# Performance work log

Hardware: AMD Instinct MI355X
Metric: run time of the kernel (lower is better)

## Reference

```python
import jax, jax.numpy as jnp
import numpy as np

TWO_PI = 2.0 * np.pi
VMIN, VMAX = 0.0, 255.0


def _reflect_idx(i, n):
    # TF fill_mode='reflect': (d c b a | a b c d | d c b a), i.e. mirror including edge
    m = jnp.mod(i, 2 * n)
    return jnp.where(m < n, m, 2 * n - 1 - m)


def _bilinear(img, sy, sx):
    # img: [H, W, C]; sy, sx: [H, W] float source coords
    H, W, _ = img.shape
    y0f = jnp.floor(sy)
    x0f = jnp.floor(sx)
    wy = (sy - y0f)[..., None]
    wx = (sx - x0f)[..., None]
    y0 = y0f.astype(jnp.int32)
    x0 = x0f.astype(jnp.int32)
    y0r = _reflect_idx(y0, H)
    y1r = _reflect_idx(y0 + 1, H)
    x0r = _reflect_idx(x0, W)
    x1r = _reflect_idx(x0 + 1, W)
    return (img[y0r, x0r] * (1 - wy) * (1 - wx)
            + img[y0r, x1r] * (1 - wy) * wx
            + img[y1r, x0r] * wy * (1 - wx)
            + img[y1r, x1r] * wy * wx)


def _affine_warp(img, a, b, c, d):
    # inverse map about image center: src = center + [[a,b],[c,d]] @ (dst - center)
    H, W, _ = img.shape
    cy = (H - 1) / 2.0
    cx = (W - 1) / 2.0
    y = jnp.arange(H, dtype=img.dtype)[:, None] - cy   # [H,1]
    x = jnp.arange(W, dtype=img.dtype)[None, :] - cx   # [1,W]
    sx = a * x + b * y + cx
    sy = c * x + d * y + cy
    return _bilinear(img, sy, sx)


def setup_inputs() -> dict:
    key = jax.random.key(0)
    k = jax.random.split(key, 7)
    B, H, W, C = 32, 512, 512, 3
    inputs = jax.random.uniform(k[0], (B, H, W, C), dtype=jnp.float32) * 255.0
    flip_h = jax.random.bernoulli(k[1], 0.5, (B,))
    flip_v = jax.random.bernoulli(k[2], 0.5, (B,))
    # RandomRotation(factor=0.5): angle in [-0.5, 0.5] * 2*pi
    angle = jax.random.uniform(k[3], (B,), jnp.float32, -0.5, 0.5) * TWO_PI
    # RandomZoom(height_factor=0.5, width_factor=None): isotropic zoom in [0.5, 1.5]
    zoom = jax.random.uniform(k[4], (B,), jnp.float32, 0.5, 1.5)
    # RandomBrightness(factor=0.5, value_range=(0,255)): delta in [-0.5, 0.5]*255
    delta = jax.random.uniform(k[5], (B,), jnp.float32, -0.5, 0.5) * 255.0
    # RandomContrast(factor=0.5): contrast multiplier in [0.5, 1.5]
    contrast = jax.random.uniform(k[6], (B,), jnp.float32, 0.5, 1.5)
    return {"inputs": inputs, "flip_h": flip_h, "flip_v": flip_v,
            "angle": angle, "zoom": zoom, "delta": delta, "contrast": contrast}


def reference(inputs, flip_h, flip_v, angle, zoom, delta, contrast):
    # 1) RandomFlip('horizontal_and_vertical'): independent per-image coin flips
    x = jnp.where(flip_h[:, None, None, None], inputs[:, :, ::-1, :], inputs)
    x = jnp.where(flip_v[:, None, None, None], x[:, ::-1, :, :], x)
    # 2) RandomRotation: bilinear warp, reflect fill
    cos = jnp.cos(angle)
    sin = jnp.sin(angle)
    x = jax.vmap(_affine_warp)(x, cos, -sin, sin, cos)
    # 3) RandomZoom (isotropic since width_factor=None): second bilinear warp
    zeros = jnp.zeros_like(zoom)
    x = jax.vmap(_affine_warp)(x, zoom, zeros, zeros, zoom)
    # 4) RandomBrightness: add per-image delta, clip to value_range
    x = jnp.clip(x + delta[:, None, None, None], VMIN, VMAX)
    # 5) RandomContrast: (x - per-channel mean) * f + mean, clip to value_range
    mean = jnp.mean(x, axis=(1, 2), keepdims=True)  # [B,1,1,C]
    x = jnp.clip((x - mean) * contrast[:, None, None, None] + mean, VMIN, VMAX)
    return x
```

## Files before the change

### kernel.cpp

```cpp
#include <hip/hip_runtime.h>


constexpr int Hh = 512, Ww = 512, Cc = 3, BATCH = 32;
constexpr int HW = Hh * Ww;
constexpr float CTR = 255.5f;
constexpr size_t IMG_FLOATS = (size_t)HW * Cc;

constexpr int TW = 64, TH = 16;
constexpr int RW = 99, RH = 26;
constexpr int KFILL = 10;

__device__ __forceinline__ int reflect1024(int i) {
    int m = i & 1023;
    return (m < 512) ? m : (1023 - m);
}

#define LOADPX(RX, RY, WX, WY, T00, T01, T10, T11)                              \
    {                                                                           \
        const int gx_ = reflect1024(rx0 + (int)(RX));                           \
        const int gy_ = reflect1024(ry0 + (int)(RY));                           \
        const float fx_ = (float)gx_ - CTR, fy_ = (float)gy_ - CTR;             \
                         \
        const float sx_ = cs * fx_ - sn * fy_ + CTR;                            \
        const float sy_ = sn * fx_ + cs * fy_ + CTR;                            \
        const float xf_ = floorf(sx_), yf_ = floorf(sy_);                       \
        (WX) = sx_ - xf_; (WY) = sy_ - yf_;                                     \
        const int xa_ = reflect1024((int)xf_)     ^ fhm;                        \
        const int xb_ = reflect1024((int)xf_ + 1) ^ fhm;                        \
        const int ya_ = reflect1024((int)yf_)     ^ fvm;                        \
        const int yb_ = reflect1024((int)yf_ + 1) ^ fvm;                        \
        (T00) = img[ya_ * Ww + xa_]; (T01) = img[ya_ * Ww + xb_];               \
        (T10) = img[yb_ * Ww + xa_]; (T11) = img[yb_ * Ww + xb_];               \
    }

#define STOREPX(RX, RY, WX, WY, T00, T01, T10, T11)                             \
    {                                                                           \
        const float w1y_ = 1.f - (WY), w1x_ = 1.f - (WX);                       \
        float3 o_;                                                              \
        o_.x = (((T00).x * w1y_) * w1x_) + (((T01).x * w1y_) * (WX))            \
             + (((T10).x * (WY)) * w1x_) + (((T11).x * (WY)) * (WX));           \
        o_.y = (((T00).y * w1y_) * w1x_) + (((T01).y * w1y_) * (WX))            \
             + (((T10).y * (WY)) * w1x_) + (((T11).y * (WY)) * (WX));           \
        o_.z = (((T00).z * w1y_) * w1x_) + (((T01).z * w1y_) * (WX))            \
             + (((T10).z * (WY)) * w1x_) + (((T11).z * (WY)) * (WX));           \
        lds[(RY)][(RX)] = o_;                                                   \
    }

__global__ __launch_bounds__(256, 4) void warp_fused(
    const float* __restrict__ in,
    const int* __restrict__ fh, const int* __restrict__ fv,
    const float* __restrict__ angle, const float* __restrict__ zoom,
    const float* __restrict__ delta,
    float* __restrict__ out, double* __restrict__ sums)
{
    __shared__ float3 lds[RH][RW];
    __shared__ float red[4][3];

    const int b = blockIdx.z;
    const float ang = angle[b];
    const float cs = cosf(ang), sn = sinf(ang);
    const float z  = zoom[b];
    const float dl = delta[b];
    const int fhm = fh[b] ? 511 : 0;
    const int fvm = fv[b] ? 511 : 0;
    const float3* __restrict__ img = (const float3*)(in + (size_t)b * IMG_FLOATS);
    float* __restrict__ outb = out + (size_t)b * IMG_FLOATS;

    const int X0 = blockIdx.x * TW;
    const int Y0 = blockIdx.y * TH;

    const int rx0 = (int)floorf(z * ((float)X0 - CTR) + CTR);
    const int ry0 = (int)floorf(z * ((float)Y0 - CTR) + CTR);
    const int rx1 = (int)floorf(z * ((float)(X0 + TW - 1) - CTR) + CTR) + 1;
    const int ry1 = (int)floorf(z * ((float)(Y0 + TH - 1) - CTR) + CTR) + 1;
    const unsigned Wr = (unsigned)(rx1 - rx0 + 1);
    const unsigned Hr = (unsigned)(ry1 - ry0 + 1);
    const unsigned N  = Wr * Hr;

    {
        unsigned i  = threadIdx.x;
        unsigned ry = i / Wr;
        unsigned rx = i - ry * Wr;
        const unsigned q = 256u / Wr;
        const unsigned r = 256u - q * Wr;

        bool cv = (i < N);
        unsigned crx = rx, cry = ry;
        float cwx, cwy; float3 c00, c01, c10, c11;
        if (cv) LOADPX(crx, cry, cwx, cwy, c00, c01, c10, c11);

        #pragma unroll
        for (int t = 1; t <= KFILL; ++t) {
            i += 256u;
            rx += r; ry += q;
            if (rx >= Wr) { rx -= Wr; ry += 1u; }
            const bool nv = (t < KFILL) && (i < N);
            unsigned nrx = rx, nry = ry;
            float nwx, nwy; float3 n00, n01, n10, n11;
            if (nv) LOADPX(nrx, nry, nwx, nwy, n00, n01, n10, n11);
            if (cv) STOREPX(crx, cry, cwx, cwy, c00, c01, c10, c11);
            cv = nv; crx = nrx; cry = nry; cwx = nwx; cwy = nwy;
            c00 = n00; c01 = n01; c10 = n10; c11 = n11;
        }
    }
    __syncthreads();

    const int tx  = threadIdx.x & 63;
    const int ty0 = threadIdx.x >> 6;
    const float sx = z * ((float)(X0 + tx) - CTR) + CTR;
    const float xf = floorf(sx);
    const float wx = sx - xf;
    const int lxa = (int)xf - rx0;
    const float w1x = 1.f - wx;

    float s0 = 0.f, s1 = 0.f, s2 = 0.f;
    #pragma unroll
    for (int k = 0; k < 4; ++k) {
        const int y = Y0 + ty0 + (k << 2);
        const float sy = z * ((float)y - CTR) + CTR;
        const float yf = floorf(sy);
        const float wy = sy - yf;
        const int lya = (int)yf - ry0;
        const float w1y = 1.f - wy;
        const float3 a0 = lds[lya][lxa],     a1 = lds[lya][lxa + 1];
        const float3 b0 = lds[lya + 1][lxa], b1 = lds[lya + 1][lxa + 1];
        float3 t;
        t.x = ((a0.x * w1y) * w1x) + ((a1.x * w1y) * wx)
            + ((b0.x * wy) * w1x)  + ((b1.x * wy) * wx);
        t.y = ((a0.y * w1y) * w1x) + ((a1.y * w1y) * wx)
            + ((b0.y * wy) * w1x)  + ((b1.y * wy) * wx);
        t.z = ((a0.z * w1y) * w1x) + ((a1.z * w1y) * wx)
            + ((b0.z * wy) * w1x)  + ((b1.z * wy) * wx);
        t.x = fminf(fmaxf(t.x + dl, 0.f), 255.f);
        t.y = fminf(fmaxf(t.y + dl, 0.f), 255.f);
        t.z = fminf(fmaxf(t.z + dl, 0.f), 255.f);
        *(float3*)(outb + (size_t)((y << 9) + X0 + tx) * 3) = t;
        s0 += t.x; s1 += t.y; s2 += t.z;
    }

    #pragma unroll
    for (int off = 32; off > 0; off >>= 1) {
        s0 += __shfl_down(s0, off);
        s1 += __shfl_down(s1, off);
        s2 += __shfl_down(s2, off);
    }
    const int lane = threadIdx.x & 63, wid = threadIdx.x >> 6;
    if (lane == 0) { red[wid][0] = s0; red[wid][1] = s1; red[wid][2] = s2; }
    __syncthreads();
    if (threadIdx.x == 0) {
        atomicAdd(&sums[b * 3 + 0], (double)red[0][0] + red[1][0] + red[2][0] + red[3][0]);
        atomicAdd(&sums[b * 3 + 1], (double)red[0][1] + red[1][1] + red[2][1] + red[3][1]);
        atomicAdd(&sums[b * 3 + 2], (double)red[0][2] + red[1][2] + red[2][2] + red[3][2]);
    }
}

__global__ __launch_bounds__(256) void contrast_pass(
    float* __restrict__ out, const double* __restrict__ sums,
    const float* __restrict__ contrast)
{
    const int b = blockIdx.y;
    const float f = contrast[b];
    const double invN = 1.0 / (double)HW;
    const float m0 = (float)(sums[b * 3 + 0] * invN);
    const float m1 = (float)(sums[b * 3 + 1] * invN);
    const float m2 = (float)(sums[b * 3 + 2] * invN);
    float4* base = reinterpret_cast<float4*>(out + (size_t)b * IMG_FLOATS);

    #pragma unroll
    for (int it = 0; it < 4; ++it) {
        const int i4 = it * 49152 + blockIdx.x * 256 + threadIdx.x;
        float4 v = base[i4];
        int c = (int)(((unsigned)i4 * 4u) % 3u);
        float m;
        m = (c == 0) ? m0 : ((c == 1) ? m1 : m2);
        v.x = fminf(fmaxf((v.x - m) * f + m, 0.f), 255.f); c = (c == 2) ? 0 : c + 1;
        m = (c == 0) ? m0 : ((c == 1) ? m1 : m2);
        v.y = fminf(fmaxf((v.y - m) * f + m, 0.f), 255.f); c = (c == 2) ? 0 : c + 1;
        m = (c == 0) ? m0 : ((c == 1) ? m1 : m2);
        v.z = fminf(fmaxf((v.z - m) * f + m, 0.f), 255.f); c = (c == 2) ? 0 : c + 1;
        m = (c == 0) ? m0 : ((c == 1) ? m1 : m2);
        v.w = fminf(fmaxf((v.w - m) * f + m, 0.f), 255.f);
        base[i4] = v;
    }
}

extern "C" void kernel_launch(void* const* d_in, const int* in_sizes, int n_in,
                              void* d_out, int out_size, void* d_ws, size_t ws_size,
                              hipStream_t stream) {
    const float* in       = (const float*)d_in[0];
    const int*   fh       = (const int*)d_in[1];
    const int*   fv       = (const int*)d_in[2];
    const float* angle    = (const float*)d_in[3];
    const float* zoom     = (const float*)d_in[4];
    const float* delta    = (const float*)d_in[5];
    const float* contrast = (const float*)d_in[6];
    float*  out  = (float*)d_out;
    double* sums = (double*)d_ws;

    hipMemsetAsync(d_ws, 0, BATCH * 3 * sizeof(double), stream);

    dim3 blk(256);
    dim3 g1(Ww / TW, Hh / TH, BATCH);
    warp_fused<<<g1, blk, 0, stream>>>(in, fh, fv, angle, zoom, delta, out, sums);

    dim3 g2(192, BATCH);
    contrast_pass<<<g2, blk, 0, stream>>>(out, sums, contrast);
}
```

Measured before the change: 306.1 us.

## Orient rotation-stage fill traversal by angle and batch two loads per iteration

The shared-memory fill of the rotated region now walks the region in row-major or column-major order, whichever matches the rotation angle, so that neighbouring threads gather from nearby source pixels and global accesses coalesce better. The fixed 10-step unrolled software pipeline is replaced by a runtime-bounded loop that issues two independent pixel loads before their stores, and out-of-range lanes are clamped to the last valid element rather than predicated off. The intent is to cut wasted iterations and improve memory locality. In exchange it adds redundant duplicate loads and stores from clamped lanes plus extra index arithmetic.

```diff
diff --git a/kernel.cpp b/kernel.cpp
--- a/kernel.cpp
+++ b/kernel.cpp
@@ -8,7 +8,6 @@
 
 constexpr int TW = 64, TH = 16;
 constexpr int RW = 99, RH = 26;
-constexpr int KFILL = 10;
 
 __device__ __forceinline__ int reflect1024(int i) {
     int m = i & 1023;
@@ -78,29 +77,41 @@
     const unsigned N  = Wr * Hr;
 
     {
-        unsigned i  = threadIdx.x;
-        unsigned ry = i / Wr;
-        unsigned rx = i - ry * Wr;
-        const unsigned q = 256u / Wr;
-        const unsigned r = 256u - q * Wr;
-
-        bool cv = (i < N);
-        unsigned crx = rx, cry = ry;
-        float cwx, cwy; float3 c00, c01, c10, c11;
-        if (cv) LOADPX(crx, cry, cwx, cwy, c00, c01, c10, c11);
-
-        #pragma unroll
-        for (int t = 1; t <= KFILL; ++t) {
-            i += 256u;
-            rx += r; ry += q;
-            if (rx >= Wr) { rx -= Wr; ry += 1u; }
-            const bool nv = (t < KFILL) && (i < N);
-            unsigned nrx = rx, nry = ry;
-            float nwx, nwy; float3 n00, n01, n10, n11;
-            if (nv) LOADPX(nrx, nry, nwx, nwy, n00, n01, n10, n11);
-            if (cv) STOREPX(crx, cry, cwx, cwy, c00, c01, c10, c11);
-            cv = nv; crx = nrx; cry = nry; cwx = nwx; cwy = nwy;
-            c00 = n00; c01 = n01; c10 = n10; c11 = n11;
+        const bool rowmajor = fabsf(sn) <= fabsf(cs);
+        const unsigned FW = rowmajor ? Wr : Hr;
+
+        unsigned iA = threadIdx.x;
+        unsigned vA = iA / FW;
+        unsigned uA = iA - vA * FW;
+        const unsigned q1 = 256u / FW, r1 = 256u - q1 * FW;
+        const unsigned q2 = 512u / FW, r2 = 512u - q2 * FW;
+        const unsigned vL = (N - 1u) / FW;
+        const unsigned uL = (N - 1u) - vL * FW;
+        const unsigned iters = (N + 511u) >> 9;
+
+        for (unsigned t = 0; t < iters; ++t) {
+            unsigned uB = uA + r1, vB = vA + q1;
+            const bool wB = (uB >= FW);
+            uB = wB ? uB - FW : uB;  vB = wB ? vB + 1u : vB;
+
+            const bool av = (iA < N);
+            const bool bv = (iA + 256u < N);
+            const unsigned ua = av ? uA : uL, va = av ? vA : vL;
+            const unsigned ub = bv ? uB : uL, vb = bv ? vB : vL;
+            const unsigned rxa = rowmajor ? ua : va, rya = rowmajor ? va : ua;
+            const unsigned rxb = rowmajor ? ub : vb, ryb = rowmajor ? vb : ub;
+
+            float wxa, wya; float3 a00, a01, a10, a11;
+            LOADPX(rxa, rya, wxa, wya, a00, a01, a10, a11);
+            float wxb, wyb; float3 b00, b01, b10, b11;
+            LOADPX(rxb, ryb, wxb, wyb, b00, b01, b10, b11);
+            STOREPX(rxa, rya, wxa, wya, a00, a01, a10, a11);
+            STOREPX(rxb, ryb, wxb, wyb, b00, b01, b10, b11);
+
+            iA += 512u;
+            unsigned uN = uA + r2, vN = vA + q2;
+            const bool wN = (uN >= FW);
+            uA = wN ? uN - FW : uN;  vA = wN ? vN + 1u : vN;
         }
     }
     __syncthreads();
```

Result: faster. 279.1 us (-8.8%).
